# Optimization experiments

Hardware: AMD Instinct MI355X
Metric: run time of the kernel (lower is better)

Reference implementation:

```python
import jax, jax.numpy as jnp
import numpy as np

B, F_IN, D_IN = 1024, 64, 64
N_CAPS, D_CAPS = 32, 64
ROUTINGS = 3
HEADS = 2
EPS = 1e-7  # K.epsilon()


def setup_inputs() -> dict:
    key = jax.random.key(0)
    ks = jax.random.split(key, 8)
    P = N_CAPS * (N_CAPS - 1) // 2
    return {
        "x": jax.random.normal(ks[0], (B, F_IN, D_IN), jnp.float32),
        "reweight_W": jax.random.normal(ks[1], (D_IN, N_CAPS, D_CAPS), jnp.float32) * 0.05,
        "routing_init": 10.0 * jax.random.truncated_normal(ks[2], -2.0, 2.0, (N_CAPS, F_IN), jnp.float32),
        "kernel_fm": jnp.full((N_CAPS, 1), 0.5, jnp.float32),
        "bias_fm": jnp.zeros((D_CAPS,), jnp.float32),
        "kernel_mf": jnp.ones((P, 1), jnp.float32),
        "bias_mf": jnp.zeros((D_CAPS,), jnp.float32),
        "kernel_highint": jnp.full((N_CAPS, 1), 0.5, jnp.float32),
        "bias_highint": jnp.zeros((D_CAPS * HEADS,), jnp.float32),
        "W_query": jax.random.normal(ks[3], (D_CAPS, D_CAPS * HEADS), jnp.float32) * 0.05,
        "W_key": jax.random.normal(ks[4], (D_CAPS, D_CAPS * HEADS), jnp.float32) * 0.05,
        "W_value": jax.random.normal(ks[5], (D_CAPS, D_CAPS * HEADS), jnp.float32) * 0.05,
        "W_res": jax.random.normal(ks[6], (D_CAPS, D_CAPS * HEADS), jnp.float32) * 0.05,
    }


def _squash(v):
    s = jnp.sum(v * v, axis=-1, keepdims=True) + EPS
    return (jnp.sqrt(s) / (0.5 + s)) * v


def _heads(t):
    # [B,N,H*F] -> [H,B,N,F] (matches tf.stack(tf.split(t, H, axis=2)))
    b, n, _ = t.shape
    return t.reshape(b, n, HEADS, D_CAPS).transpose(2, 0, 1, 3)


def reference(x, reweight_W, routing_init, kernel_fm, bias_fm, kernel_mf, bias_mf,
              kernel_highint, bias_highint, W_query, W_key, W_value, W_res):
    # inputs_hat: [B, N, F, C]
    inputs_hat = jnp.einsum('bfd,dnc->bnfc', x, reweight_W)
    b_logits = jnp.broadcast_to(routing_init[None], (x.shape[0], N_CAPS, F_IN))
    for _ in range(ROUTINGS):
        c = jax.nn.softmax(b_logits, axis=1)            # softmax over capsules
        outputs = _squash(jnp.einsum('bnf,bnfc->bnc', c, inputs_hat))
        b_logits = b_logits + jnp.einsum('bnc,bnfc->bnf', outputs, inputs_hat)
    c = jax.nn.softmax(b_logits, axis=1)
    routing_score = c[..., None]                        # [B,N,F,1]
    attention_output = routing_score * inputs_hat       # [B,N,F,C]

    # FM per-field: square-of-sum minus sum-of-square over input capsules
    sum_f = jnp.sum(attention_output, axis=2)           # [B,N,C]
    field_fm = sum_f ** 2 - jnp.sum(attention_output ** 2, axis=2)
    hi_fm = jnp.sum(field_fm * kernel_fm[None], axis=1) + bias_fm  # [B,C]

    field_wise_vectors = sum_f                          # [B,N,C]

    # pairwise MF interactions (itertools.combinations order == triu indices)
    li, ri = np.triu_indices(N_CAPS, k=1)
    emb_prod = field_wise_vectors[:, li] * field_wise_vectors[:, ri]  # [B,P,C]
    h_mf = jnp.sum(emb_prod * kernel_mf[None], axis=1) + bias_mf      # [B,C]

    # InteractingLayer (multi-head self-attention over fields, use_res=True)
    q = _heads(jnp.einsum('bnd,de->bne', field_wise_vectors, W_query))  # [H,B,N,F]
    k = _heads(jnp.einsum('bnd,de->bne', field_wise_vectors, W_key))
    v = _heads(jnp.einsum('bnd,de->bne', field_wise_vectors, W_value))
    attn = jax.nn.softmax(jnp.einsum('hbnf,hbmf->hbnm', q, k), axis=-1)
    out = jnp.einsum('hbnm,hbmf->hbnf', attn, v)        # [H,B,N,F]
    out = out.transpose(1, 2, 0, 3).reshape(x.shape[0], N_CAPS, HEADS * D_CAPS)
    res = jnp.einsum('bnd,de->bne', field_wise_vectors, W_res)
    fv2 = jax.nn.relu(out + res)                        # [B,N,H*F]
    high_int = jnp.sum(fv2 * kernel_highint[None], axis=1) + bias_highint  # [B,2C]

    return jnp.concatenate([hi_fm, h_mf, high_int], axis=-1), routing_score
```

## Files before the change

### kernel.cpp

```cpp
#include <hip/hip_runtime.h>


#define EPS_SQ 1e-7f

typedef __attribute__((ext_vector_type(8))) short bf16x8;
typedef __attribute__((ext_vector_type(4))) float floatx4;

__device__ __forceinline__ int lidx(int r, int c) {
  return r * 68 + ((((c >> 2) ^ (r >> 2)) & 15) << 2) + (c & 3);
}
__device__ __forceinline__ unsigned short f2bf(float f) {
  unsigned u = __float_as_uint(f);
  u += 0x7FFFu + ((u >> 16) & 1u);
  return (unsigned short)(u >> 16);
}

__global__ __launch_bounds__(256) void k_prep2(
    const float* __restrict__ W, const float* __restrict__ Wq,
    const float* __restrict__ Wk, const float* __restrict__ kmf,
    float* __restrict__ Qb, float* __restrict__ Ab, float* __restrict__ Kb)
{
  const int t = threadIdx.x;
  if (blockIdx.x < 32) {
    __shared__ __align__(16) float Mn[64 * 68];
    const int n = blockIdx.x;
#pragma unroll
    for (int k = 0; k < 4; k++) {
      int lin = t + 256 * k; int d = lin >> 4; int c0 = (lin & 15) << 2;
      *(float4*)&Mn[lidx(d, c0)] = *(const float4*)(W + d * 2048 + n * 64 + c0);
    }
    __syncthreads();
    const int d1 = (t >> 4) * 4, d2 = (t & 15) * 4;
    float acc[4][4] = {};
    for (int cq = 0; cq < 64; cq += 4) {
      float m1[4][4], m2[4][4];
#pragma unroll
      for (int i = 0; i < 4; i++) *(float4*)m1[i] = *(const float4*)&Mn[lidx(d1 + i, cq)];
#pragma unroll
      for (int j = 0; j < 4; j++) *(float4*)m2[j] = *(const float4*)&Mn[lidx(d2 + j, cq)];
#pragma unroll
      for (int i = 0; i < 4; i++)
#pragma unroll
        for (int j = 0; j < 4; j++) {
          float s = 0.f;
#pragma unroll
          for (int k = 0; k < 4; k++) s += m1[i][k] * m2[j][k];
          acc[i][j] += s;
        }
    }
#pragma unroll
    for (int i = 0; i < 4; i++)
      *(float4*)(Qb + n * 4096 + (d1 + i) * 64 + d2) = *(float4*)acc[i];
  } else if (blockIdx.x < 40) {
    __shared__ __align__(16) float wkS[64 * 68];
    __shared__ __align__(16) float wqS[16 * 68];
    const int hb = blockIdx.x - 32;
    const int h = hb & 1, rg = hb >> 1;
#pragma unroll
    for (int k = 0; k < 4; k++) {
      int lin = t + 256 * k; int dp = lin >> 4; int e0 = (lin & 15) << 2;
      *(float4*)&wkS[lidx(dp, e0)] = *(const float4*)(Wk + dp * 128 + h * 64 + e0);
    }
    {
      int dl = t >> 4, e0 = (t & 15) << 2;
      *(float4*)&wqS[lidx(dl, e0)] = *(const float4*)(Wq + (rg * 16 + dl) * 128 + h * 64 + e0);
    }
    __syncthreads();
    const int dl = t >> 4, dp0 = (t & 15) << 2;
    float acc[4] = {};
    for (int e = 0; e < 64; e += 4) {
      float q4[4];
      *(float4*)q4 = *(const float4*)&wqS[lidx(dl, e)];
#pragma unroll
      for (int c = 0; c < 4; c++) {
        float mr[4];
        *(float4*)mr = *(const float4*)&wkS[lidx(dp0 + c, e)];
        acc[c] += q4[0] * mr[0] + q4[1] * mr[1] + q4[2] * mr[2] + q4[3] * mr[3];
      }
    }
    *(float4*)(Ab + h * 4096 + (rg * 16 + dl) * 64 + dp0) = *(float4*)acc;
  } else {
    __shared__ float Ks[1024];
    *(float4*)&Ks[t * 4] = make_float4(0.f, 0.f, 0.f, 0.f);
    __syncthreads();
    if (t < 248) {
#pragma unroll
      for (int j = 0; j < 2; j++) {
        int p = t * 2 + j;
        if (p < 496) {
          int l = 0, rem = p;
          while (rem >= 31 - l) { rem -= 31 - l; ++l; }
          int r = l + 1 + rem;
          float v = kmf[p];
          Ks[l * 32 + r] = v;
          Ks[r * 32 + l] = v;
        }
      }
    }
    __syncthreads();
    *(float4*)&Kb[t * 4] = *(const float4*)&Ks[t * 4];
  }
}

__global__ __launch_bounds__(256) void k_route2(
    const float* __restrict__ x, const float* __restrict__ W,
    const float* __restrict__ rinit, const float* __restrict__ Qb,
    float* __restrict__ rs, float* __restrict__ fwv)
{
  __shared__ __align__(16) float xs[64 * 68];
  __shared__ __align__(16) float bS[32 * 68];
  __shared__ __align__(16) float cS[32 * 68];
  __shared__ __align__(16) float xcS[32 * 68];
  __shared__ __align__(16) float owS[32 * 68];
  const int b = blockIdx.x, t = threadIdx.x;
  const int tn = t >> 4, tlo = t & 15;
  const int nq = t >> 3, sub = t & 7;

#pragma unroll
  for (int k = 0; k < 4; k++) {
    int lin = t + 256 * k; int f = lin >> 4; int d0 = (lin & 15) << 2;
    *(float4*)&xs[lidx(f, d0)] = *(const float4*)(x + b * 4096 + f * 64 + d0);
  }
#pragma unroll
  for (int k = 0; k < 2; k++) {
    int lin = t + 256 * k; int n = lin >> 4; int f0 = (lin & 15) << 2;
    *(float4*)&bS[lidx(n, f0)] = *(const float4*)(rinit + n * 64 + f0);
  }
  __syncthreads();

  for (int it = 0; it < 4; it++) {
    {
      const int nl = t & 31, fg = t >> 5;
#pragma unroll
      for (int k = 0; k < 8; k++) {
        int f = fg * 8 + k;
        float v = bS[lidx(nl, f)];
        float m = v;
        for (int s = 16; s > 0; s >>= 1) m = fmaxf(m, __shfl_xor(m, s, 64));
        float e = __expf(v - m);
        float sum = e;
        for (int s = 16; s > 0; s >>= 1) sum += __shfl_xor(sum, s, 64);
        cS[lidx(nl, f)] = e / sum;
      }
    }
    __syncthreads();
    if (it == 3) {
#pragma unroll
      for (int k = 0; k < 8; k++) {
        int lin = t + 256 * k; int n = lin >> 6, f = lin & 63;
        rs[b * 2048 + n * 64 + f] = cS[lidx(n, f)];
      }
    }
    {
      const int n0 = tn * 2, d0 = tlo * 4;
      float acc[2][4] = {{0, 0, 0, 0}, {0, 0, 0, 0}};
      for (int f = 0; f < 64; f++) {
        float c0v = cS[lidx(n0, f)];
        float c1v = cS[lidx(n0 + 1, f)];
        float xr[4];
        *(float4*)xr = *(const float4*)&xs[lidx(f, d0)];
#pragma unroll
        for (int i = 0; i < 4; i++) {
          acc[0][i] += c0v * xr[i];
          acc[1][i] += c1v * xr[i];
        }
      }
      *(float4*)&xcS[lidx(n0, d0)] = *(float4*)acc[0];
      *(float4*)&xcS[lidx(n0 + 1, d0)] = *(float4*)acc[1];
    }
    __syncthreads();
    if (it == 3) break;

    {
      const float* Qn = Qb + nq * 4096 + sub * 8;
      float y[8] = {};
#pragma unroll 4
      for (int d1 = 0; d1 < 64; d1++) {
        float xv = xcS[lidx(nq, d1)];
        float4 qa = *(const float4*)(Qn + d1 * 64);
        float4 qb2 = *(const float4*)(Qn + d1 * 64 + 4);
        y[0] += xv * qa.x; y[1] += xv * qa.y; y[2] += xv * qa.z; y[3] += xv * qa.w;
        y[4] += xv * qb2.x; y[5] += xv * qb2.y; y[6] += xv * qb2.z; y[7] += xv * qb2.w;
      }
      float xa[4], xb2[4];
      *(float4*)xa = *(const float4*)&xcS[lidx(nq, sub * 8)];
      *(float4*)xb2 = *(const float4*)&xcS[lidx(nq, sub * 8 + 4)];
      float ps = y[0] * xa[0] + y[1] * xa[1] + y[2] * xa[2] + y[3] * xa[3]
               + y[4] * xb2[0] + y[5] * xb2[1] + y[6] * xb2[2] + y[7] * xb2[3];
      ps += __shfl_xor(ps, 1, 64);
      ps += __shfl_xor(ps, 2, 64);
      ps += __shfl_xor(ps, 4, 64);
      const float ss = ps + EPS_SQ;
      const float sc = sqrtf(ss) / (0.5f + ss);
      float o0[4] = {y[0] * sc, y[1] * sc, y[2] * sc, y[3] * sc};
      float o1[4] = {y[4] * sc, y[5] * sc, y[6] * sc, y[7] * sc};
      *(float4*)&owS[lidx(nq, sub * 8)] = *(float4*)o0;
      *(float4*)&owS[lidx(nq, sub * 8 + 4)] = *(float4*)o1;
    }
    __syncthreads();

    {
      const int n0 = tn * 2, f0 = tlo * 4;
      float acc[2][4] = {{0, 0, 0, 0}, {0, 0, 0, 0}};
      for (int dq = 0; dq < 64; dq += 4) {
        float o[2][4];
        *(float4*)o[0] = *(const float4*)&owS[lidx(n0, dq)];
        *(float4*)o[1] = *(const float4*)&owS[lidx(n0 + 1, dq)];
#pragma unroll
        for (int i = 0; i < 4; i++) {
          float xr[4];
          *(float4*)xr = *(const float4*)&xs[lidx(f0 + i, dq)];
#pragma unroll
          for (int k = 0; k < 4; k++) {
            acc[0][i] += o[0][k] * xr[k];
            acc[1][i] += o[1][k] * xr[k];
          }
        }
      }
#pragma unroll
      for (int j = 0; j < 2; j++) {
        float tmp[4];
        *(float4*)tmp = *(const float4*)&bS[lidx(n0 + j, f0)];
#pragma unroll
        for (int i = 0; i < 4; i++) tmp[i] += acc[j][i];
        *(float4*)&bS[lidx(n0 + j, f0)] = *(float4*)tmp;
      }
    }
    __syncthreads();
  }

  {
    const float* Wn = W + nq * 64 + sub * 8;
    float a8[8] = {};
#pragma unroll 4
    for (int d = 0; d < 64; d++) {
      float xv = xcS[lidx(nq, d)];
      float4 wa = *(const float4*)(Wn + d * 2048);
      float4 wb = *(const float4*)(Wn + d * 2048 + 4);
      a8[0] += xv * wa.x; a8[1] += xv * wa.y; a8[2] += xv * wa.z; a8[3] += xv * wa.w;
      a8[4] += xv * wb.x; a8[5] += xv * wb.y; a8[6] += xv * wb.z; a8[7] += xv * wb.w;
    }
    float o0[4] = {a8[0], a8[1], a8[2], a8[3]};
    float o1[4] = {a8[4], a8[5], a8[6], a8[7]};
    *(float4*)(fwv + b * 2048 + nq * 64 + sub * 8) = *(float4*)o0;
    *(float4*)(fwv + b * 2048 + nq * 64 + sub * 8 + 4) = *(float4*)o1;
  }
}

__global__ __launch_bounds__(256) void k_ih(
    const float* __restrict__ x, const float* __restrict__ W,
    const float* __restrict__ rs, float* __restrict__ ssq)
{
  __shared__ __align__(16) unsigned short xB[4 * 64 * 64];
  __shared__ __align__(16) unsigned short wB[2 * 64 * 64];
  __shared__ unsigned short cF2[4 * 8 * 64];
  const int n_oct = (blockIdx.x & 3) << 3, b0 = (blockIdx.x >> 2) * 4;
  const int t = threadIdx.x, w = t >> 6, lane = t & 63;

#pragma unroll
  for (int k = 0; k < 16; k++) {
    int ch = t + 256 * k;
    int bb = ch >> 10, rem = ch & 1023;
    int f = rem >> 4, fq = rem & 15;
    int dg = fq >> 1, half = fq & 1;
    float4 v = *(const float4*)(x + ((b0 + bb) * 64 + f) * 64 + fq * 4);
    unsigned p0 = f2bf(v.x) | ((unsigned)f2bf(v.y) << 16);
    unsigned p1 = f2bf(v.z) | ((unsigned)f2bf(v.w) << 16);
    *(uint2*)&xB[bb * 4096 + f * 64 + ((dg ^ (f & 7)) << 3) + half * 4] =
        make_uint2(p0, p1);
  }
#pragma unroll
  for (int nn = 0; nn < 8; nn++) {
    float v = rs[(b0 + w) * 2048 + (n_oct + nn) * 64 + lane];
    cF2[(w * 8 + nn) * 64 + lane] = f2bf(v * v);
  }
  __syncthreads();

  const int m = lane & 15, q = lane >> 4, ms = m & 7;
  bf16x8 a[4][2];
#pragma unroll
  for (int mi = 0; mi < 4; mi++) {
    const unsigned short* bp = xB + w * 4096 + (mi * 16 + m) * 64;
#pragma unroll
    for (int kk = 0; kk < 2; kk++)
      a[mi][kk] = *(const bf16x8*)&bp[((kk * 4 + q) ^ ms) << 3];
  }

  for (int np = 0; np < 4; np++) {
    const int n0 = n_oct + np * 2;
    __syncthreads();
    {
      int dd = t >> 2, cq = t & 3;
      int dg = dd >> 3, dl = dd & 7;
#pragma unroll
      for (int nn = 0; nn < 2; nn++) {
        const float* wp = W + dd * 2048 + (n0 + nn) * 64 + cq * 16;
        unsigned short* base = wB + nn * 4096;
#pragma unroll
        for (int i4 = 0; i4 < 4; i4++) {
          float4 v = *(const float4*)(wp + i4 * 4);
          float vv[4] = {v.x, v.y, v.z, v.w};
#pragma unroll
          for (int j = 0; j < 4; j++) {
            int c = cq * 16 + i4 * 4 + j;
            base[c * 64 + ((dg ^ (c & 7)) << 3) + dl] = f2bf(vv[j]);
          }
        }
      }
    }
    __syncthreads();
#pragma unroll
    for (int nn = 0; nn < 2; nn++) {
      bf16x8 bf[4][2];
#pragma unroll
      for (int ci = 0; ci < 4; ci++) {
        const unsigned short* bp = wB + nn * 4096 + (ci * 16 + m) * 64;
#pragma unroll
        for (int kk = 0; kk < 2; kk++)
          bf[ci][kk] = *(const bf16x8*)&bp[((kk * 4 + q) ^ ms) << 3];
      }
      float ps[4] = {0.f, 0.f, 0.f, 0.f};
      const unsigned short* cf = cF2 + (w * 8 + np * 2 + nn) * 64 + q * 4;
#pragma unroll
      for (int mi = 0; mi < 4; mi++) {
        float cfv[4];
#pragma unroll
        for (int r = 0; r < 4; r++)
          cfv[r] = __uint_as_float((unsigned)cf[mi * 16 + r] << 16);
#pragma unroll
        for (int ci = 0; ci < 4; ci++) {
          floatx4 c0 = {0.f, 0.f, 0.f, 0.f};
          c0 = __builtin_amdgcn_mfma_f32_16x16x32_bf16(a[mi][0], bf[ci][0], c0, 0, 0, 0);
          c0 = __builtin_amdgcn_mfma_f32_16x16x32_bf16(a[mi][1], bf[ci][1], c0, 0, 0, 0);
#pragma unroll
          for (int r = 0; r < 4; r++) { float tv = c0[r]; ps[ci] += cfv[r] * tv * tv; }
        }
      }
#pragma unroll
      for (int ci = 0; ci < 4; ci++) {
        ps[ci] += __shfl_xor(ps[ci], 16, 64);
        ps[ci] += __shfl_xor(ps[ci], 32, 64);
      }
      if (q == 0) {
#pragma unroll
        for (int ci = 0; ci < 4; ci++)
          ssq[(b0 + w) * 2048 + (n0 + nn) * 64 + ci * 16 + m] = ps[ci];
      }
    }
  }
}

__global__ __launch_bounds__(256) void k_attn(
    const float* __restrict__ fwv, const float* __restrict__ ssq,
    const float* __restrict__ Ab, const float* __restrict__ Kb,
    const float* __restrict__ Wv, const float* __restrict__ Wr,
    const float* __restrict__ kfm, const float* __restrict__ bfm,
    const float* __restrict__ bmf, const float* __restrict__ khi,
    const float* __restrict__ bhi, float* __restrict__ out0)
{
  __shared__ __align__(16) float smem[8832];
  float* fwS  = smem;
  float* pS   = smem + 2176;
  float* bufA = smem + 4480;
  float* tS   = smem + 6656;
  float* vS   = smem + 4480;
  float* redH = smem + 2176;
  float* Kf   = smem + 4480;
  float* red1 = smem + 5504;

  const int b = blockIdx.x, t = threadIdx.x;
  const int tn = t >> 4, te = t & 15;
  const int n0 = tn * 2, e0 = te * 8, d0 = te * 4;

#pragma unroll
  for (int k = 0; k < 2; k++) {
    int lin = t + 256 * k; int nn = lin >> 4; int c0 = (lin & 15) << 2;
    *(float4*)&fwS[lidx(nn, c0)] = *(const float4*)(fwv + b * 2048 + nn * 64 + c0);
  }
  __syncthreads();

  for (int h = 0; h < 2; h++) {
    float tacc[2][4] = {};
    for (int half = 0; half < 2; half++) {
#pragma unroll
      for (int k = 0; k < 2; k++) {
        int lin = t + 256 * k; int d = lin >> 4; int c0 = (lin & 15) << 2;
        *(float4*)&bufA[lidx(d, c0)] =
            *(const float4*)(Ab + h * 4096 + (half * 32 + d) * 64 + c0);
      }
      __syncthreads();
      for (int dq = 0; dq < 32; dq += 4) {
        float fw0[4], fw1[4];
        *(float4*)fw0 = *(const float4*)&fwS[lidx(n0, half * 32 + dq)];
        *(float4*)fw1 = *(const float4*)&fwS[lidx(n0 + 1, half * 32 + dq)];
#pragma unroll
        for (int j = 0; j < 4; j++) {
          float mr[4];
          *(float4*)mr = *(const float4*)&bufA[lidx(dq + j, d0)];
#pragma unroll
          for (int c = 0; c < 4; c++) {
            tacc[0][c] += fw0[j] * mr[c];
            tacc[1][c] += fw1[j] * mr[c];
          }
        }
      }
      __syncthreads();
    }
    *(float4*)&tS[lidx(n0, d0)] = *(float4*)tacc[0];
    *(float4*)&tS[lidx(n0 + 1, d0)] = *(float4*)tacc[1];
    __syncthreads();
    {
      const int m0 = te * 2;
      float s00 = 0.f, s01 = 0.f, s10 = 0.f, s11 = 0.f;
      for (int kk = 0; kk < 16; kk++) {
        float ta0[4], ta1[4], f0[4], f1[4];
        *(float4*)ta0 = *(const float4*)&tS[lidx(n0, kk * 4)];
        *(float4*)ta1 = *(const float4*)&tS[lidx(n0 + 1, kk * 4)];
        *(float4*)f0 = *(const float4*)&fwS[lidx(m0, kk * 4)];
        *(float4*)f1 = *(const float4*)&fwS[lidx(m0 + 1, kk * 4)];
#pragma unroll
        for (int j = 0; j < 4; j++) {
          s00 += ta0[j] * f0[j]; s01 += ta0[j] * f1[j];
          s10 += ta1[j] * f0[j]; s11 += ta1[j] * f1[j];
        }
      }
      pS[(h * 32 + n0) * 36 + m0] = s00;
      pS[(h * 32 + n0) * 36 + m0 + 1] = s01;
      pS[(h * 32 + n0 + 1) * 36 + m0] = s10;
      pS[(h * 32 + n0 + 1) * 36 + m0 + 1] = s11;
    }
    __syncthreads();
  }

  {
    const int r = t >> 2, sub = t & 3;
    const int base = r * 36 + sub * 8;
    float v0[4], v1[4];
    *(float4*)v0 = *(const float4*)&pS[base];
    *(float4*)v1 = *(const float4*)&pS[base + 4];
    float mx = fmaxf(fmaxf(fmaxf(v0[0], v0[1]), fmaxf(v0[2], v0[3])),
                     fmaxf(fmaxf(v1[0], v1[1]), fmaxf(v1[2], v1[3])));
    mx = fmaxf(mx, __shfl_xor(mx, 1, 64));
    mx = fmaxf(mx, __shfl_xor(mx, 2, 64));
    float sum = 0.f;
#pragma unroll
    for (int j = 0; j < 4; j++) { v0[j] = __expf(v0[j] - mx); sum += v0[j]; }
#pragma unroll
    for (int j = 0; j < 4; j++) { v1[j] = __expf(v1[j] - mx); sum += v1[j]; }
    sum += __shfl_xor(sum, 1, 64);
    sum += __shfl_xor(sum, 2, 64);
    const float inv = 1.0f / sum;
#pragma unroll
    for (int j = 0; j < 4; j++) { v0[j] *= inv; v1[j] *= inv; }
    *(float4*)&pS[base] = *(float4*)v0;
    *(float4*)&pS[base + 4] = *(float4*)v1;
  }
  __syncthreads();

  {
    float acc[2][8] = {};
    for (int dq = 0; dq < 64; dq += 4) {
      float fw0[4], fw1[4];
      *(float4*)fw0 = *(const float4*)&fwS[lidx(n0, dq)];
      *(float4*)fw1 = *(const float4*)&fwS[lidx(n0 + 1, dq)];
#pragma unroll
      for (int jj = 0; jj < 4; jj++) {
        float w8[8];
        *(float4*)&w8[0] = *(const float4*)(Wv + (dq + jj) * 128 + e0);
        *(float4*)&w8[4] = *(const float4*)(Wv + (dq + jj) * 128 + e0 + 4);
#pragma unroll
        for (int j = 0; j < 8; j++) {
          acc[0][j] += fw0[jj] * w8[j];
          acc[1][j] += fw1[jj] * w8[j];
        }
      }
    }
    *(float4*)&vS[n0 * 132 + e0] = *(float4*)&acc[0][0];
    *(float4*)&vS[n0 * 132 + e0 + 4] = *(float4*)&acc[0][4];
    *(float4*)&vS[(n0 + 1) * 132 + e0] = *(float4*)&acc[1][0];
    *(float4*)&vS[(n0 + 1) * 132 + e0 + 4] = *(float4*)&acc[1][4];
  }
  __syncthreads();

  {
    const int h2 = te >> 3;
    float pacc[2][8] = {};
    for (int m = 0; m < 32; m++) {
      float p0 = pS[(h2 * 32 + n0) * 36 + m];
      float p1 = pS[(h2 * 32 + n0 + 1) * 36 + m];
      float vr[8];
      *(float4*)&vr[0] = *(const float4*)&vS[m * 132 + e0];
      *(float4*)&vr[4] = *(const float4*)&vS[m * 132 + e0 + 4];
#pragma unroll
      for (int j = 0; j < 8; j++) {
        pacc[0][j] += p0 * vr[j];
        pacc[1][j] += p1 * vr[j];
      }
    }
    for (int dq = 0; dq < 64; dq += 4) {
      float fw0[4], fw1[4];
      *(float4*)fw0 = *(const float4*)&fwS[lidx(n0, dq)];
      *(float4*)fw1 = *(const float4*)&fwS[lidx(n0 + 1, dq)];
#pragma unroll
      for (int jj = 0; jj < 4; jj++) {
        float w8[8];
        *(float4*)&w8[0] = *(const float4*)(Wr + (dq + jj) * 128 + e0);
        *(float4*)&w8[4] = *(const float4*)(Wr + (dq + jj) * 128 + e0 + 4);
#pragma unroll
        for (int j = 0; j < 8; j++) {
          pacc[0][j] += fw0[jj] * w8[j];
          pacc[1][j] += fw1[jj] * w8[j];
        }
      }
    }
    __syncthreads();
    {
      float kh0 = khi[n0], kh1 = khi[n0 + 1];
      float ph[8];
#pragma unroll
      for (int j = 0; j < 8; j++)
        ph[j] = kh0 * fmaxf(pacc[0][j], 0.f) + kh1 * fmaxf(pacc[1][j], 0.f);
      *(float4*)&redH[tn * 132 + e0] = *(float4*)&ph[0];
      *(float4*)&redH[tn * 132 + e0 + 4] = *(float4*)&ph[4];
    }
  }
  *(float4*)&Kf[t * 4] = *(const float4*)(Kb + t * 4);
  __syncthreads();

  if (t < 128) {
    float s = 0.f;
#pragma unroll
    for (int k = 0; k < 16; k++) s += redH[k * 132 + t];
    out0[b * 256 + 128 + t] = s + bhi[t];
  }
  {
    const int c = t & 63, nq = t >> 6;
    float p = 0.f;
#pragma unroll
    for (int k = 0; k < 8; k++) {
      int nn = nq * 8 + k;
      float fv = fwS[lidx(nn, c)];
      float sv = ssq[b * 2048 + nn * 64 + c];
      p += (fv * fv - sv) * kfm[nn];
    }
    red1[nq * 68 + c] = p;
    float inner[8] = {};
    for (int r = 0; r < 32; r++) {
      float fr = fwS[lidx(r, c)];
#pragma unroll
      for (int l8 = 0; l8 < 8; l8++)
        inner[l8] += Kf[(nq * 8 + l8) * 32 + r] * fr;
    }
    float hmf = 0.f;
#pragma unroll
    for (int l8 = 0; l8 < 8; l8++)
      hmf += fwS[lidx(nq * 8 + l8, c)] * inner[l8];
    red1[(4 + nq) * 68 + c] = hmf;
  }
  __syncthreads();
  if (t < 64) {
    out0[b * 256 + t] = red1[t] + red1[68 + t] + red1[136 + t] + red1[204 + t] + bfm[t];
    float h2 = red1[272 + t] + red1[340 + t] + red1[408 + t] + red1[476 + t];
    out0[b * 256 + 64 + t] = 0.5f * h2 + bmf[t];
  }
}

extern "C" void kernel_launch(void* const* d_in, const int* in_sizes, int n_in,
                              void* d_out, int out_size, void* d_ws, size_t ws_size,
                              hipStream_t stream) {
  (void)in_sizes; (void)n_in; (void)out_size; (void)ws_size;
  const float* x     = (const float*)d_in[0];
  const float* W     = (const float*)d_in[1];
  const float* rinit = (const float*)d_in[2];
  const float* kfm   = (const float*)d_in[3];
  const float* bfm   = (const float*)d_in[4];
  const float* kmf   = (const float*)d_in[5];
  const float* bmf   = (const float*)d_in[6];
  const float* khi   = (const float*)d_in[7];
  const float* bhi   = (const float*)d_in[8];
  const float* Wq    = (const float*)d_in[9];
  const float* Wk    = (const float*)d_in[10];
  const float* Wv    = (const float*)d_in[11];
  const float* Wr    = (const float*)d_in[12];

  float* out0 = (float*)d_out;
  float* rs   = out0 + 1024 * 256;

  float* ws   = (float*)d_ws;
  float* Abuf = ws;
  float* Kbuf = ws + 8192;
  float* Qbuf = ws + 16384;
  float* fwv  = ws + 2097152;
  float* ssq  = ws + 2 * 2097152;

  k_prep2<<<41, 256, 0, stream>>>(W, Wq, Wk, kmf, Qbuf, Abuf, Kbuf);
  k_route2<<<1024, 256, 0, stream>>>(x, W, rinit, Qbuf, rs, fwv);
  k_ih<<<1024, 256, 0, stream>>>(x, W, rs, ssq);
  k_attn<<<1024, 256, 0, stream>>>(fwv, ssq, Abuf, Kbuf, Wv, Wr,
                                   kfm, bfm, bmf, khi, bhi, out0);
}
```

Baseline: 272.1 us.

## Process two batch rows per routing block to share Q and W global loads

The routing kernel now handles two batch elements per 512-thread block. In the squash/Q-projection and the final W-projection, each thread computes the same output columns for both batch rows, so every Q or W float4 read from global memory is reused twice. Shared memory is compacted by aliasing the softmax-coefficient and squashed-output buffers and switching to an unpadded XOR-swizzled 64-wide layout. This halves redundant weight traffic but enlarges the block, which may reduce occupancy and adds more block-wide barriers across twice as many threads.

After: 273.2 us. About the same (+0.4%).

```diff
diff --git a/kernel.cpp b/kernel.cpp
--- a/kernel.cpp
+++ b/kernel.cpp
@@ -8,6 +8,9 @@
 
 __device__ __forceinline__ int lidx(int r, int c) {
   return r * 68 + ((((c >> 2) ^ (r >> 2)) & 15) << 2) + (c & 3);
+}
+__device__ __forceinline__ int lidx64(int r, int c) {
+  return r * 64 + ((((c >> 2) ^ r) & 15) << 2) + (c & 3);
 }
 __device__ __forceinline__ unsigned short f2bf(float f) {
   unsigned u = __float_as_uint(f);
@@ -102,100 +105,112 @@
   }
 }
 
-__global__ __launch_bounds__(256) void k_route2(
+__global__ __launch_bounds__(512, 4) void k_route3(
     const float* __restrict__ x, const float* __restrict__ W,
     const float* __restrict__ rinit, const float* __restrict__ Qb,
     float* __restrict__ rs, float* __restrict__ fwv)
 {
-  __shared__ __align__(16) float xs[64 * 68];
-  __shared__ __align__(16) float bS[32 * 68];
-  __shared__ __align__(16) float cS[32 * 68];
-  __shared__ __align__(16) float xcS[32 * 68];
-  __shared__ __align__(16) float owS[32 * 68];
-  const int b = blockIdx.x, t = threadIdx.x;
-  const int tn = t >> 4, tlo = t & 15;
-  const int nq = t >> 3, sub = t & 7;
+  __shared__ __align__(16) float smem[2 * 10240];
+
+  const int t = threadIdx.x;
+  const int tb = t >> 8, tt = t & 255;
+  const int b = blockIdx.x * 2 + tb;
+
+  float* xs  = smem + tb * 10240;
+  float* bS  = smem + tb * 10240 + 4096;
+  float* cOw = smem + tb * 10240 + 6144;
+  float* xcS = smem + tb * 10240 + 8192;
+
+  float* xc0 = smem + 8192;
+  float* xc1 = smem + 10240 + 8192;
+  float* ow0 = smem + 6144;
+  float* ow1 = smem + 10240 + 6144;
 
 #pragma unroll
   for (int k = 0; k < 4; k++) {
-    int lin = t + 256 * k; int f = lin >> 4; int d0 = (lin & 15) << 2;
-    *(float4*)&xs[lidx(f, d0)] = *(const float4*)(x + b * 4096 + f * 64 + d0);
+    int lin = tt + 256 * k; int f = lin >> 4; int d0 = (lin & 15) << 2;
+    *(float4*)&xs[lidx64(f, d0)] = *(const float4*)(x + b * 4096 + f * 64 + d0);
   }
 #pragma unroll
   for (int k = 0; k < 2; k++) {
-    int lin = t + 256 * k; int n = lin >> 4; int f0 = (lin & 15) << 2;
-    *(float4*)&bS[lidx(n, f0)] = *(const float4*)(rinit + n * 64 + f0);
+    int lin = tt + 256 * k; int n = lin >> 4; int f0 = (lin & 15) << 2;
+    *(float4*)&bS[lidx64(n, f0)] = *(const float4*)(rinit + n * 64 + f0);
   }
   __syncthreads();
 
+  const int tn = tt >> 4, tlo = tt & 15;
+  const int nq = t >> 4, sub = t & 15;
+
   for (int it = 0; it < 4; it++) {
     {
-      const int nl = t & 31, fg = t >> 5;
+      const int nl = tt & 31, fg = tt >> 5;
 #pragma unroll
       for (int k = 0; k < 8; k++) {
         int f = fg * 8 + k;
-        float v = bS[lidx(nl, f)];
+        float v = bS[lidx64(nl, f)];
         float m = v;
         for (int s = 16; s > 0; s >>= 1) m = fmaxf(m, __shfl_xor(m, s, 64));
         float e = __expf(v - m);
         float sum = e;
         for (int s = 16; s > 0; s >>= 1) sum += __shfl_xor(sum, s, 64);
-        cS[lidx(nl, f)] = e / sum;
+        cOw[lidx64(nl, f)] = e / sum;
       }
     }
     __syncthreads();
     if (it == 3) {
 #pragma unroll
       for (int k = 0; k < 8; k++) {
-        int lin = t + 256 * k; int n = lin >> 6, f = lin & 63;
-        rs[b * 2048 + n * 64 + f] = cS[lidx(n, f)];
+        int lin = tt + 256 * k; int n = lin >> 6, f = lin & 63;
+        rs[b * 2048 + n * 64 + f] = cOw[lidx64(n, f)];
       }
     }
     {
       const int n0 = tn * 2, d0 = tlo * 4;
       float acc[2][4] = {{0, 0, 0, 0}, {0, 0, 0, 0}};
       for (int f = 0; f < 64; f++) {
-        float c0v = cS[lidx(n0, f)];
-        float c1v = cS[lidx(n0 + 1, f)];
+        float c0v = cOw[lidx64(n0, f)];
+        float c1v = cOw[lidx64(n0 + 1, f)];
         float xr[4];
-        *(float4*)xr = *(const float4*)&xs[lidx(f, d0)];
+        *(float4*)xr = *(const float4*)&xs[lidx64(f, d0)];
 #pragma unroll
         for (int i = 0; i < 4; i++) {
           acc[0][i] += c0v * xr[i];
           acc[1][i] += c1v * xr[i];
         }
       }
-      *(float4*)&xcS[lidx(n0, d0)] = *(float4*)acc[0];
-      *(float4*)&xcS[lidx(n0 + 1, d0)] = *(float4*)acc[1];
+      *(float4*)&xcS[lidx64(n0, d0)] = *(float4*)acc[0];
+      *(float4*)&xcS[lidx64(n0 + 1, d0)] = *(float4*)acc[1];
     }
     __syncthreads();
     if (it == 3) break;
 
     {
-      const float* Qn = Qb + nq * 4096 + sub * 8;
-      float y[8] = {};
+      const float* Qn = Qb + nq * 4096 + sub * 4;
+      float y0[4] = {}, y1[4] = {};
 #pragma unroll 4
       for (int d1 = 0; d1 < 64; d1++) {
-        float xv = xcS[lidx(nq, d1)];
-        float4 qa = *(const float4*)(Qn + d1 * 64);
-        float4 qb2 = *(const float4*)(Qn + d1 * 64 + 4);
-        y[0] += xv * qa.x; y[1] += xv * qa.y; y[2] += xv * qa.z; y[3] += xv * qa.w;
-        y[4] += xv * qb2.x; y[5] += xv * qb2.y; y[6] += xv * qb2.z; y[7] += xv * qb2.w;
-      }
-      float xa[4], xb2[4];
-      *(float4*)xa = *(const float4*)&xcS[lidx(nq, sub * 8)];
-      *(float4*)xb2 = *(const float4*)&xcS[lidx(nq, sub * 8 + 4)];
-      float ps = y[0] * xa[0] + y[1] * xa[1] + y[2] * xa[2] + y[3] * xa[3]
-               + y[4] * xb2[0] + y[5] * xb2[1] + y[6] * xb2[2] + y[7] * xb2[3];
-      ps += __shfl_xor(ps, 1, 64);
-      ps += __shfl_xor(ps, 2, 64);
-      ps += __shfl_xor(ps, 4, 64);
-      const float ss = ps + EPS_SQ;
-      const float sc = sqrtf(ss) / (0.5f + ss);
-      float o0[4] = {y[0] * sc, y[1] * sc, y[2] * sc, y[3] * sc};
-      float o1[4] = {y[4] * sc, y[5] * sc, y[6] * sc, y[7] * sc};
-      *(float4*)&owS[lidx(nq, sub * 8)] = *(float4*)o0;
-      *(float4*)&owS[lidx(nq, sub * 8 + 4)] = *(float4*)o1;
+        float xv0 = xc0[lidx64(nq, d1)];
+        float xv1 = xc1[lidx64(nq, d1)];
+        float4 q = *(const float4*)(Qn + d1 * 64);
+        y0[0] += xv0 * q.x; y0[1] += xv0 * q.y; y0[2] += xv0 * q.z; y0[3] += xv0 * q.w;
+        y1[0] += xv1 * q.x; y1[1] += xv1 * q.y; y1[2] += xv1 * q.z; y1[3] += xv1 * q.w;
+      }
+      float xa0[4], xa1[4];
+      *(float4*)xa0 = *(const float4*)&xc0[lidx64(nq, sub * 4)];
+      *(float4*)xa1 = *(const float4*)&xc1[lidx64(nq, sub * 4)];
+      float ps0 = y0[0] * xa0[0] + y0[1] * xa0[1] + y0[2] * xa0[2] + y0[3] * xa0[3];
+      float ps1 = y1[0] * xa1[0] + y1[1] * xa1[1] + y1[2] * xa1[2] + y1[3] * xa1[3];
+      ps0 += __shfl_xor(ps0, 1, 64); ps0 += __shfl_xor(ps0, 2, 64);
+      ps0 += __shfl_xor(ps0, 4, 64); ps0 += __shfl_xor(ps0, 8, 64);
+      ps1 += __shfl_xor(ps1, 1, 64); ps1 += __shfl_xor(ps1, 2, 64);
+      ps1 += __shfl_xor(ps1, 4, 64); ps1 += __shfl_xor(ps1, 8, 64);
+      const float ss0 = ps0 + EPS_SQ, ss1 = ps1 + EPS_SQ;
+      const float sc0 = sqrtf(ss0) / (0.5f + ss0);
+      const float sc1 = sqrtf(ss1) / (0.5f + ss1);
+      float o0[4] = {y0[0] * sc0, y0[1] * sc0, y0[2] * sc0, y0[3] * sc0};
+      float o1[4] = {y1[0] * sc1, y1[1] * sc1, y1[2] * sc1, y1[3] * sc1};
+      *(float4*)&ow0[lidx64(nq, sub * 4)] = *(float4*)o0;
+      *(float4*)&ow1[lidx64(nq, sub * 4)] = *(float4*)o1;
     }
     __syncthreads();
 
@@ -204,12 +219,12 @@
       float acc[2][4] = {{0, 0, 0, 0}, {0, 0, 0, 0}};
       for (int dq = 0; dq < 64; dq += 4) {
         float o[2][4];
-        *(float4*)o[0] = *(const float4*)&owS[lidx(n0, dq)];
-        *(float4*)o[1] = *(const float4*)&owS[lidx(n0 + 1, dq)];
+        *(float4*)o[0] = *(const float4*)&cOw[lidx64(n0, dq)];
+        *(float4*)o[1] = *(const float4*)&cOw[lidx64(n0 + 1, dq)];
 #pragma unroll
         for (int i = 0; i < 4; i++) {
           float xr[4];
-          *(float4*)xr = *(const float4*)&xs[lidx(f0 + i, dq)];
+          *(float4*)xr = *(const float4*)&xs[lidx64(f0 + i, dq)];
 #pragma unroll
           for (int k = 0; k < 4; k++) {
             acc[0][i] += o[0][k] * xr[k];
@@ -220,30 +235,29 @@
 #pragma unroll
       for (int j = 0; j < 2; j++) {
         float tmp[4];
-        *(float4*)tmp = *(const float4*)&bS[lidx(n0 + j, f0)];
+        *(float4*)tmp = *(const float4*)&bS[lidx64(n0 + j, f0)];
 #pragma unroll
         for (int i = 0; i < 4; i++) tmp[i] += acc[j][i];
-        *(float4*)&bS[lidx(n0 + j, f0)] = *(float4*)tmp;
+        *(float4*)&bS[lidx64(n0 + j, f0)] = *(float4*)tmp;
       }
     }
     __syncthreads();
   }
 
   {
-    const float* Wn = W + nq * 64 + sub * 8;
-    float a8[8] = {};
+    const float* Wn = W + nq * 64 + sub * 4;
+    float a0[4] = {}, a1[4] = {};
 #pragma unroll 4
     for (int d = 0; d < 64; d++) {
-      float xv = xcS[lidx(nq, d)];
-      float4 wa = *(const float4*)(Wn + d * 2048);
-      float4 wb = *(const float4*)(Wn + d * 2048 + 4);
-      a8[0] += xv * wa.x; a8[1] += xv * wa.y; a8[2] += xv * wa.z; a8[3] += xv * wa.w;
-      a8[4] += xv * wb.x; a8[5] += xv * wb.y; a8[6] += xv * wb.z; a8[7] += xv * wb.w;
-    }
-    float o0[4] = {a8[0], a8[1], a8[2], a8[3]};
-    float o1[4] = {a8[4], a8[5], a8[6], a8[7]};
-    *(float4*)(fwv + b * 2048 + nq * 64 + sub * 8) = *(float4*)o0;
-    *(float4*)(fwv + b * 2048 + nq * 64 + sub * 8 + 4) = *(float4*)o1;
+      float xv0 = xc0[lidx64(nq, d)];
+      float xv1 = xc1[lidx64(nq, d)];
+      float4 w = *(const float4*)(Wn + d * 2048);
+      a0[0] += xv0 * w.x; a0[1] += xv0 * w.y; a0[2] += xv0 * w.z; a0[3] += xv0 * w.w;
+      a1[0] += xv1 * w.x; a1[1] += xv1 * w.y; a1[2] += xv1 * w.z; a1[3] += xv1 * w.w;
+    }
+    const int b0g = blockIdx.x * 2;
+    *(float4*)(fwv + b0g * 2048 + nq * 64 + sub * 4) = *(float4*)a0;
+    *(float4*)(fwv + (b0g + 1) * 2048 + nq * 64 + sub * 4) = *(float4*)a1;
   }
 }
 
@@ -594,7 +608,7 @@
   float* ssq  = ws + 2 * 2097152;
 
   k_prep2<<<41, 256, 0, stream>>>(W, Wq, Wk, kmf, Qbuf, Abuf, Kbuf);
-  k_route2<<<1024, 256, 0, stream>>>(x, W, rinit, Qbuf, rs, fwv);
+  k_route3<<<512, 512, 0, stream>>>(x, W, rinit, Qbuf, rs, fwv);
   k_ih<<<1024, 256, 0, stream>>>(x, W, rs, ssq);
   k_attn<<<1024, 256, 0, stream>>>(fwv, ssq, Abuf, Kbuf, Wv, Wr,
                                    kfm, bfm, bmf, khi, bhi, out0);
```
